# Kernel tuning notes

Hardware: AMD Instinct MI355X
Metric: run time of the kernel (lower is better)

## Reference

```python
import jax, jax.numpy as jnp
import numpy as np

B, C, H, W = 8, 3, 768, 1024
SAMPLE_RATIO = 0.15
G = int(H * W * SAMPLE_RATIO)  # 117964 point triplets
DELTA_COS = 0.867
DELTA_DIFF = 0.005  # hardcoded in select_points_groups' filter_mask call
DELTA_Z = 1e-4


def setup_inputs() -> dict:
    key = jax.random.key(0)
    ks = jax.random.split(key, 8)
    gt = jax.random.normal(ks[0], (B, C, H, W), dtype=jnp.float32)
    pred = jax.random.normal(ks[1], (B, C, H, W), dtype=jnp.float32)
    idx = {}
    for i, (nm, hi) in enumerate([("p1_x", W), ("p1_y", H), ("p2_x", W),
                                  ("p2_y", H), ("p3_x", W), ("p3_y", H)]):
        idx[nm] = jax.random.randint(ks[2 + i], (G,), 0, hi, dtype=jnp.int32)
    return {"gt": gt, "pred": pred, **idx}


def _form_groups(pw, p1_x, p1_y, p2_x, p2_y, p3_x, p3_y):
    # pw: [B,H,W,3] -> groups [B,G,3coord,3pts]
    g1 = pw[:, p1_y, p1_x, :]
    g2 = pw[:, p2_y, p2_x, :]
    g3 = pw[:, p3_y, p3_x, :]
    return jnp.stack([g1, g2, g3], axis=3)


def _vn_loss(gt, pred, p1_x, p1_y, p2_x, p2_y, p3_x, p3_y):
    pw_gt = jnp.transpose(gt, (0, 2, 3, 1))    # [B,H,W,3]
    pw_pred = jnp.transpose(pred, (0, 2, 3, 1))

    pw_g = _form_groups(pw_gt, p1_x, p1_y, p2_x, p2_y, p3_x, p3_y)  # [B,G,3,3]

    # pairwise difference vectors: 12, 13, 23 -> [B,G,3coord,3pair]
    pw12 = pw_g[..., 1] - pw_g[..., 0]
    pw13 = pw_g[..., 2] - pw_g[..., 0]
    pw23 = pw_g[..., 2] - pw_g[..., 1]
    pw_diff = jnp.stack([pw12, pw13, pw23], axis=3)

    # cosine-similarity (Gram) filter: energy[b,g,i,j] = <diff_i, diff_j>
    energy = jnp.einsum("bgci,bgcj->bgij", pw_diff, pw_diff)
    norms = jnp.sqrt(jnp.sum(pw_diff * pw_diff, axis=2))  # [B,G,3]
    nm = norms[..., :, None] * norms[..., None, :]
    norm_energy = energy / (nm + 1e-8)
    mask_cos = jnp.sum((norm_energy > DELTA_COS) | (norm_energy < -DELTA_COS),
                       axis=(2, 3)) > 3                   # [B,G]

    mask_pad = jnp.sum(pw_g[:, :, 2, :] > DELTA_Z, axis=2) == 3
    mask_x = jnp.sum(jnp.abs(pw_diff[:, :, 0, :]) < DELTA_DIFF, axis=2) > 0
    mask_y = jnp.sum(jnp.abs(pw_diff[:, :, 1, :]) < DELTA_DIFF, axis=2) > 0
    mask_z = jnp.sum(jnp.abs(pw_diff[:, :, 2, :]) < DELTA_DIFF, axis=2) > 0
    mask = mask_pad & ~((mask_x & mask_y & mask_z) | mask_cos)  # [B,G]

    pw_gp = _form_groups(pw_pred, p1_x, p1_y, p2_x, p2_y, p3_x, p3_y)
    # torch quirk: boolean mask over [B,G,3] (z of each point) indexes the
    # first 3 dims [B,G,coord], zeroing whole coord-rows to 1e-4
    zmask = pw_gp[:, :, 2, :] == 0.0
    pw_gp = jnp.where(zmask[:, :, :, None], 1e-4, pw_gp)

    def normals(groups):
        p12 = groups[..., 1] - groups[..., 0]
        p13 = groups[..., 2] - groups[..., 0]
        n = jnp.cross(p12, p13, axis=2)
        norm = jnp.linalg.norm(n, axis=2, keepdims=True)
        norm = norm + jnp.where(norm == 0.0, 0.01, 0.0)
        return n / norm

    gt_n = normals(pw_g)
    dt_n = normals(pw_gp)

    per_group = jnp.sum(jnp.abs(gt_n - dt_n), axis=2)  # [B,G]
    m = mask.astype(per_group.dtype)
    # mean over selected groups (batch dims flattened by the torch reshape)
    return jnp.sum(per_group * m) / jnp.maximum(jnp.sum(m), 1.0)


def reference(gt, pred, p1_x, p1_y, p2_x, p2_y, p3_x, p3_y):
    return _vn_loss(gt, pred, p1_x, p1_y, p2_x, p2_y, p3_x, p3_y)
```

## Files before the change

### kernel.cpp

```cpp
#include <hip/hip_runtime.h>
#include <hip/hip_fp16.h>

#define HW_ (768 * 1024)
#define W_ 1024
#define DC 0.867f
#define DD 0.005f
#define DZ 0.0001f

#define SEG_STRIDE 260

__device__ __forceinline__ void vn_group_math(
    const float G1[3], const float G2[3], const float G3[3],
    const float P1[3], const float P2[3], const float P3[3],
    float& s_loss, float& s_cnt)
{
    float d0[3], d1[3], d2[3];
    #pragma unroll
    for (int c = 0; c < 3; c++) {
        d0[c] = G2[c] - G1[c];
        d1[c] = G3[c] - G1[c];
        d2[c] = G3[c] - G2[c];
    }

    float e00 = d0[0]*d0[0] + d0[1]*d0[1] + d0[2]*d0[2];
    float e11 = d1[0]*d1[0] + d1[1]*d1[1] + d1[2]*d1[2];
    float e22 = d2[0]*d2[0] + d2[1]*d2[1] + d2[2]*d2[2];
    float e01 = d0[0]*d1[0] + d0[1]*d1[1] + d0[2]*d1[2];
    float e02 = d0[0]*d2[0] + d0[1]*d2[1] + d0[2]*d2[2];
    float e12 = d1[0]*d2[0] + d1[1]*d2[1] + d1[2]*d2[2];
    float s0 = sqrtf(e00), s1 = sqrtf(e11), s2 = sqrtf(e22);

    int cc = 0;
    {
        float ne;
        ne = e00 / (s0*s0 + 1e-8f); cc += (ne > DC) || (ne < -DC);
        ne = e11 / (s1*s1 + 1e-8f); cc += (ne > DC) || (ne < -DC);
        ne = e22 / (s2*s2 + 1e-8f); cc += (ne > DC) || (ne < -DC);
        ne = e01 / (s0*s1 + 1e-8f); cc += 2 * ((ne > DC) || (ne < -DC));
        ne = e02 / (s0*s2 + 1e-8f); cc += 2 * ((ne > DC) || (ne < -DC));
        ne = e12 / (s1*s2 + 1e-8f); cc += 2 * ((ne > DC) || (ne < -DC));
    }
    bool mask_cos = cc > 3;
    bool mask_pad = (G1[2] > DZ) && (G2[2] > DZ) && (G3[2] > DZ);
    bool mx = (fabsf(d0[0]) < DD) || (fabsf(d1[0]) < DD) || (fabsf(d2[0]) < DD);
    bool my = (fabsf(d0[1]) < DD) || (fabsf(d1[1]) < DD) || (fabsf(d2[1]) < DD);
    bool mz = (fabsf(d0[2]) < DD) || (fabsf(d1[2]) < DD) || (fabsf(d2[2]) < DD);
    bool mask = mask_pad && !((mx && my && mz) || mask_cos);

    if (mask) {
        float n0 = d0[1]*d1[2] - d0[2]*d1[1];
        float n1 = d0[2]*d1[0] - d0[0]*d1[2];
        float n2 = d0[0]*d1[1] - d0[1]*d1[0];
        float nn = sqrtf(n0*n0 + n1*n1 + n2*n2);
        if (nn == 0.f) nn = 0.01f;

        bool zm[3] = { P1[2] == 0.f, P2[2] == 0.f, P3[2] == 0.f };
        float Q1[3], Q2[3], Q3[3];
        #pragma unroll
        for (int c = 0; c < 3; c++) {
            Q1[c] = zm[c] ? 0.0001f : P1[c];
            Q2[c] = zm[c] ? 0.0001f : P2[c];
            Q3[c] = zm[c] ? 0.0001f : P3[c];
        }
        float q0[3], q1[3];
        #pragma unroll
        for (int c = 0; c < 3; c++) {
            q0[c] = Q2[c] - Q1[c];
            q1[c] = Q3[c] - Q1[c];
        }
        float m0 = q0[1]*q1[2] - q0[2]*q1[1];
        float m1 = q0[2]*q1[0] - q0[0]*q1[2];
        float m2 = q0[0]*q1[1] - q0[1]*q1[0];
        float mn = sqrtf(m0*m0 + m1*m1 + m2*m2);
        if (mn == 0.f) mn = 0.01f;

        s_loss += fabsf(n0/nn - m0/mn) + fabsf(n1/nn - m1/mn) + fabsf(n2/nn - m2/mn);
        s_cnt  += 1.f;
    }
}

__device__ __forceinline__ void vn_reduce_store(float s_loss, float s_cnt, double* acc)
{
    #pragma unroll
    for (int off = 32; off > 0; off >>= 1) {
        s_loss += __shfl_down(s_loss, off);
        s_cnt  += __shfl_down(s_cnt,  off);
    }
    __shared__ float ls[4], lc[4];
    int lane = threadIdx.x & 63;
    int wid  = threadIdx.x >> 6;
    if (lane == 0) { ls[wid] = s_loss; lc[wid] = s_cnt; }
    __syncthreads();
    if (threadIdx.x == 0) {
        float tl = ls[0] + ls[1] + ls[2] + ls[3];
        float tc = lc[0] + lc[1] + lc[2] + lc[3];
        atomicAdd(acc,     (double)tl);
        atomicAdd(acc + 1, (double)tc);
    }
}

__global__ __launch_bounds__(256) void vn_mark8(
    const int* __restrict__ p1x, const int* __restrict__ p1y,
    const int* __restrict__ p2x, const int* __restrict__ p2y,
    const int* __restrict__ p3x, const int* __restrict__ p3y,
    int G, unsigned char* __restrict__ mask8)
{
    int g = blockIdx.x * 256 + threadIdx.x;
    if (g >= G) return;
    mask8[p1y[g] * W_ + p1x[g]] = 1;
    mask8[p2y[g] * W_ + p2x[g]] = 1;
    mask8[p3y[g] * W_ + p3x[g]] = 1;
}

__global__ __launch_bounds__(256) void vn_pack_m(
    const float* __restrict__ gt, const float* __restrict__ pred,
    const unsigned char* __restrict__ mask8, uint4* __restrict__ rec)
{
    __shared__ __half lh[48 * SEG_STRIDE];
    __shared__ unsigned char lmask[256];

    size_t px_base = (size_t)blockIdx.x * 256;
    int t = threadIdx.x;
    int w = t >> 6, l = t & 63;

    if (t < 64)
        ((unsigned int*)lmask)[t] = ((const unsigned int*)(mask8 + px_base))[t];

    #pragma unroll
    for (int k = 0; k < 12; k++) {
        int s = w * 12 + k;
        int b = s / 6, c = s % 6;
        const float* src = (c < 3)
            ? gt   + ((size_t)b * 3 + c)       * HW_ + px_base
            : pred + ((size_t)b * 3 + (c - 3)) * HW_ + px_base;
        float4 v = *(const float4*)(src + l * 4);
        __half2 v01 = __floats2half2_rn(v.x, v.y);
        __half2 v23 = __floats2half2_rn(v.z, v.w);
        uint2 pk;
        pk.x = *(unsigned int*)&v01;
        pk.y = *(unsigned int*)&v23;
        *(uint2*)(&lh[(size_t)s * SEG_STRIDE + l * 4]) = pk;
    }

    __syncthreads();

    int b  = t & 7;
    int c6 = b * 6;
    uint4* out = rec + px_base * 8;
    #pragma unroll
    for (int r = 0; r < 8; r++) {
        int j    = t + r * 256;
        int i_px = j >> 3;
        if (lmask[i_px]) {
            uint4 o;
            __half2* hh = (__half2*)&o;
            hh[0] = __halves2half2(lh[(c6 + 0) * SEG_STRIDE + i_px],
                                   lh[(c6 + 1) * SEG_STRIDE + i_px]);
            hh[1] = __halves2half2(lh[(c6 + 2) * SEG_STRIDE + i_px],
                                   lh[(c6 + 3) * SEG_STRIDE + i_px]);
            hh[2] = __halves2half2(lh[(c6 + 4) * SEG_STRIDE + i_px],
                                   lh[(c6 + 5) * SEG_STRIDE + i_px]);
            o.w = 0u;
            out[j] = o;
        }
    }
}

__device__ __forceinline__ void unpack_rec(uint4 r, float G[3], float P[3])
{
    __half2 a = *(__half2*)&r.x;
    __half2 b = *(__half2*)&r.y;
    __half2 c = *(__half2*)&r.z;
    G[0] = __low2float(a);  G[1] = __high2float(a);
    G[2] = __low2float(b);  P[0] = __high2float(b);
    P[1] = __low2float(c);  P[2] = __high2float(c);
}

__global__ __launch_bounds__(256) void vn_gather_h(
    const uint4* __restrict__ rec,
    const int* __restrict__ p1x, const int* __restrict__ p1y,
    const int* __restrict__ p2x, const int* __restrict__ p2y,
    const int* __restrict__ p3x, const int* __restrict__ p3y,
    int G, double* __restrict__ acc)
{
    int t = blockIdx.x * 256 + threadIdx.x;
    int g = t >> 1;
    int h = (t & 1) * 4;

    float s_loss = 0.f, s_cnt = 0.f;

    if (g < G) {
        size_t q1 = ((size_t)(p1y[g] * W_ + p1x[g])) * 8 + h;
        size_t q2 = ((size_t)(p2y[g] * W_ + p2x[g])) * 8 + h;
        size_t q3 = ((size_t)(p3y[g] * W_ + p3x[g])) * 8 + h;

        uint4 r1[4], r2[4], r3[4];
        #pragma unroll
        for (int j = 0; j < 4; j++) r1[j] = rec[q1 + j];
        #pragma unroll
        for (int j = 0; j < 4; j++) r2[j] = rec[q2 + j];
        #pragma unroll
        for (int j = 0; j < 4; j++) r3[j] = rec[q3 + j];

        #pragma unroll
        for (int j = 0; j < 4; j++) {
            float G1[3], P1[3], G2[3], P2[3], G3[3], P3[3];
            unpack_rec(r1[j], G1, P1);
            unpack_rec(r2[j], G2, P2);
            unpack_rec(r3[j], G3, P3);
            vn_group_math(G1, G2, G3, P1, P2, P3, s_loss, s_cnt);
        }
    }

    vn_reduce_store(s_loss, s_cnt, acc);
}

__global__ __launch_bounds__(256) void vn_main(
    const float* __restrict__ gt, const float* __restrict__ pred,
    const int* __restrict__ p1x, const int* __restrict__ p1y,
    const int* __restrict__ p2x, const int* __restrict__ p2y,
    const int* __restrict__ p3x, const int* __restrict__ p3y,
    int G, double* __restrict__ acc)
{
    int g = blockIdx.x * 256 + threadIdx.x;
    int b = blockIdx.y;

    float s_loss = 0.f, s_cnt = 0.f;

    if (g < G) {
        int o1 = p1y[g] * W_ + p1x[g];
        int o2 = p2y[g] * W_ + p2x[g];
        int o3 = p3y[g] * W_ + p3x[g];
        const float* gb = gt   + (size_t)b * 3 * HW_;
        const float* pb = pred + (size_t)b * 3 * HW_;

        float G1[3], G2[3], G3[3], P1[3], P2[3], P3[3];
        #pragma unroll
        for (int c = 0; c < 3; c++) {
            G1[c] = gb[c * HW_ + o1];
            G2[c] = gb[c * HW_ + o2];
            G3[c] = gb[c * HW_ + o3];
            P1[c] = pb[c * HW_ + o1];
            P2[c] = pb[c * HW_ + o2];
            P3[c] = pb[c * HW_ + o3];
        }
        vn_group_math(G1, G2, G3, P1, P2, P3, s_loss, s_cnt);
    }

    vn_reduce_store(s_loss, s_cnt, acc);
}

__global__ void vn_final(const double* __restrict__ acc, float* __restrict__ out)
{
    float s = (float)acc[0];
    float c = (float)acc[1];
    out[0] = s / fmaxf(c, 1.0f);
}

extern "C" void kernel_launch(void* const* d_in, const int* in_sizes, int n_in,
                              void* d_out, int out_size, void* d_ws, size_t ws_size,
                              hipStream_t stream) {
    const float* gt   = (const float*)d_in[0];
    const float* pred = (const float*)d_in[1];
    const int* p1x = (const int*)d_in[2];
    const int* p1y = (const int*)d_in[3];
    const int* p2x = (const int*)d_in[4];
    const int* p2y = (const int*)d_in[5];
    const int* p3x = (const int*)d_in[6];
    const int* p3y = (const int*)d_in[7];

    int G = in_sizes[2];
    int B = in_sizes[0] / (3 * HW_);
    double* acc = (double*)d_ws;

    hipMemsetAsync(acc, 0, 2 * sizeof(double), stream);

    size_t mask_off   = 256;
    size_t mask_bytes = HW_;
    size_t rec_off    = 1 << 20;
    size_t rec_bytes  = (size_t)HW_ * 8 * sizeof(uint4);
    size_t need = rec_off + rec_bytes;

    if (B == 8 && ws_size >= need) {
        unsigned char* mask8 = (unsigned char*)d_ws + mask_off;
        uint4*         rec   = (uint4*)((char*)d_ws + rec_off);

        hipMemsetAsync(mask8, 0, mask_bytes, stream);
        vn_mark8<<<(G + 255) / 256, 256, 0, stream>>>(p1x, p1y, p2x, p2y, p3x, p3y, G, mask8);
        vn_pack_m<<<HW_ / 256, 256, 0, stream>>>(gt, pred, mask8, rec);
        int nthreads = G * 2;
        vn_gather_h<<<(nthreads + 255) / 256, 256, 0, stream>>>(
            rec, p1x, p1y, p2x, p2y, p3x, p3y, G, acc);
    } else {
        dim3 grid((G + 255) / 256, B);
        vn_main<<<grid, 256, 0, stream>>>(gt, pred, p1x, p1y, p2x, p2y, p3x, p3y, G, acc);
    }

    vn_final<<<1, 1, 0, stream>>>(acc, (float*)d_out);
}
```

Measured before the change: 78.99 us.

## Split packed per-pixel records into 8-byte and 4-byte arrays, fold acc reset

Each per-pixel-per-batch record was a 16-byte uint4 with 4 bytes of padding. It is now split into an 8-byte array and a 4-byte array, so the gather kernel reads 12 bytes per record instead of 16, through wider vector loads. The zeroing of the accumulator moves from a separate memset into the mark kernel, which saves one launch. The trade-off is that the gather now issues three separate load streams per point, and the acc reset depends on kernel ordering within the stream.

```diff
diff --git a/kernel.cpp b/kernel.cpp
--- a/kernel.cpp
+++ b/kernel.cpp
@@ -103,9 +103,13 @@
     const int* __restrict__ p1x, const int* __restrict__ p1y,
     const int* __restrict__ p2x, const int* __restrict__ p2y,
     const int* __restrict__ p3x, const int* __restrict__ p3y,
-    int G, unsigned char* __restrict__ mask8)
+    int G, unsigned char* __restrict__ mask8, double* __restrict__ acc)
 {
     int g = blockIdx.x * 256 + threadIdx.x;
+    if (blockIdx.x == 0 && threadIdx.x == 0) {
+        acc[0] = 0.0;
+        acc[1] = 0.0;
+    }
     if (g >= G) return;
     mask8[p1y[g] * W_ + p1x[g]] = 1;
     mask8[p2y[g] * W_ + p2x[g]] = 1;
@@ -114,7 +118,8 @@
 
 __global__ __launch_bounds__(256) void vn_pack_m(
     const float* __restrict__ gt, const float* __restrict__ pred,
-    const unsigned char* __restrict__ mask8, uint4* __restrict__ rec)
+    const unsigned char* __restrict__ mask8,
+    uint2* __restrict__ recLo, unsigned int* __restrict__ recHi)
 {
     __shared__ __half lh[48 * SEG_STRIDE];
     __shared__ unsigned char lmask[256];
@@ -146,38 +151,41 @@
 
     int b  = t & 7;
     int c6 = b * 6;
-    uint4* out = rec + px_base * 8;
+    uint2*        outLo = recLo + px_base * 8;
+    unsigned int* outHi = recHi + px_base * 8;
     #pragma unroll
     for (int r = 0; r < 8; r++) {
         int j    = t + r * 256;
         int i_px = j >> 3;
         if (lmask[i_px]) {
-            uint4 o;
-            __half2* hh = (__half2*)&o;
-            hh[0] = __halves2half2(lh[(c6 + 0) * SEG_STRIDE + i_px],
-                                   lh[(c6 + 1) * SEG_STRIDE + i_px]);
-            hh[1] = __halves2half2(lh[(c6 + 2) * SEG_STRIDE + i_px],
-                                   lh[(c6 + 3) * SEG_STRIDE + i_px]);
-            hh[2] = __halves2half2(lh[(c6 + 4) * SEG_STRIDE + i_px],
-                                   lh[(c6 + 5) * SEG_STRIDE + i_px]);
-            o.w = 0u;
-            out[j] = o;
-        }
-    }
-}
-
-__device__ __forceinline__ void unpack_rec(uint4 r, float G[3], float P[3])
-{
-    __half2 a = *(__half2*)&r.x;
-    __half2 b = *(__half2*)&r.y;
-    __half2 c = *(__half2*)&r.z;
+            __half2 w0 = __halves2half2(lh[(c6 + 0) * SEG_STRIDE + i_px],
+                                        lh[(c6 + 1) * SEG_STRIDE + i_px]);
+            __half2 w1 = __halves2half2(lh[(c6 + 2) * SEG_STRIDE + i_px],
+                                        lh[(c6 + 3) * SEG_STRIDE + i_px]);
+            __half2 w2 = __halves2half2(lh[(c6 + 4) * SEG_STRIDE + i_px],
+                                        lh[(c6 + 5) * SEG_STRIDE + i_px]);
+            uint2 lo;
+            lo.x = *(unsigned int*)&w0;
+            lo.y = *(unsigned int*)&w1;
+            outLo[j] = lo;
+            outHi[j] = *(unsigned int*)&w2;
+        }
+    }
+}
+
+__device__ __forceinline__ void unpack_s(unsigned int lo0, unsigned int lo1,
+                                         unsigned int hi, float G[3], float P[3])
+{
+    __half2 a = *(__half2*)&lo0;
+    __half2 b = *(__half2*)&lo1;
+    __half2 c = *(__half2*)&hi;
     G[0] = __low2float(a);  G[1] = __high2float(a);
     G[2] = __low2float(b);  P[0] = __high2float(b);
     P[1] = __low2float(c);  P[2] = __high2float(c);
 }
 
-__global__ __launch_bounds__(256) void vn_gather_h(
-    const uint4* __restrict__ rec,
+__global__ __launch_bounds__(256) void vn_gather_s(
+    const uint2* __restrict__ recLo, const unsigned int* __restrict__ recHi,
     const int* __restrict__ p1x, const int* __restrict__ p1y,
     const int* __restrict__ p2x, const int* __restrict__ p2y,
     const int* __restrict__ p3x, const int* __restrict__ p3y,
@@ -194,20 +202,29 @@
         size_t q2 = ((size_t)(p2y[g] * W_ + p2x[g])) * 8 + h;
         size_t q3 = ((size_t)(p3y[g] * W_ + p3x[g])) * 8 + h;
 
-        uint4 r1[4], r2[4], r3[4];
-        #pragma unroll
-        for (int j = 0; j < 4; j++) r1[j] = rec[q1 + j];
-        #pragma unroll
-        for (int j = 0; j < 4; j++) r2[j] = rec[q2 + j];
-        #pragma unroll
-        for (int j = 0; j < 4; j++) r3[j] = rec[q3 + j];
+        const uint4* L = (const uint4*)recLo;
+        const uint4* H = (const uint4*)recHi;
+
+        uint4 a1 = L[q1 >> 1], b1 = L[(q1 >> 1) + 1], h1 = H[q1 >> 2];
+        uint4 a2 = L[q2 >> 1], b2 = L[(q2 >> 1) + 1], h2v = H[q2 >> 2];
+        uint4 a3 = L[q3 >> 1], b3 = L[(q3 >> 1) + 1], h3 = H[q3 >> 2];
+
+        unsigned int lo0_1[4] = {a1.x, a1.z, b1.x, b1.z};
+        unsigned int lo1_1[4] = {a1.y, a1.w, b1.y, b1.w};
+        unsigned int hi_1[4]  = {h1.x, h1.y, h1.z, h1.w};
+        unsigned int lo0_2[4] = {a2.x, a2.z, b2.x, b2.z};
+        unsigned int lo1_2[4] = {a2.y, a2.w, b2.y, b2.w};
+        unsigned int hi_2[4]  = {h2v.x, h2v.y, h2v.z, h2v.w};
+        unsigned int lo0_3[4] = {a3.x, a3.z, b3.x, b3.z};
+        unsigned int lo1_3[4] = {a3.y, a3.w, b3.y, b3.w};
+        unsigned int hi_3[4]  = {h3.x, h3.y, h3.z, h3.w};
 
         #pragma unroll
         for (int j = 0; j < 4; j++) {
             float G1[3], P1[3], G2[3], P2[3], G3[3], P3[3];
-            unpack_rec(r1[j], G1, P1);
-            unpack_rec(r2[j], G2, P2);
-            unpack_rec(r3[j], G3, P3);
+            unpack_s(lo0_1[j], lo1_1[j], hi_1[j], G1, P1);
+            unpack_s(lo0_2[j], lo1_2[j], hi_2[j], G2, P2);
+            unpack_s(lo0_3[j], lo1_3[j], hi_3[j], G3, P3);
             vn_group_math(G1, G2, G3, P1, P2, P3, s_loss, s_cnt);
         }
     }
@@ -271,27 +288,30 @@
 
     int G = in_sizes[2];
     int B = in_sizes[0] / (3 * HW_);
+
     double* acc = (double*)d_ws;
 
-    hipMemsetAsync(acc, 0, 2 * sizeof(double), stream);
-
-    size_t mask_off   = 256;
-    size_t mask_bytes = HW_;
-    size_t rec_off    = 1 << 20;
-    size_t rec_bytes  = (size_t)HW_ * 8 * sizeof(uint4);
-    size_t need = rec_off + rec_bytes;
+    size_t mask_off  = 256;
+    size_t lo_off    = 1 << 20;
+    size_t lo_bytes  = (size_t)HW_ * 8 * sizeof(uint2);
+    size_t hi_off    = lo_off + lo_bytes;
+    size_t hi_bytes  = (size_t)HW_ * 8 * sizeof(unsigned int);
+    size_t need = hi_off + hi_bytes;
 
     if (B == 8 && ws_size >= need) {
         unsigned char* mask8 = (unsigned char*)d_ws + mask_off;
-        uint4*         rec   = (uint4*)((char*)d_ws + rec_off);
-
-        hipMemsetAsync(mask8, 0, mask_bytes, stream);
-        vn_mark8<<<(G + 255) / 256, 256, 0, stream>>>(p1x, p1y, p2x, p2y, p3x, p3y, G, mask8);
-        vn_pack_m<<<HW_ / 256, 256, 0, stream>>>(gt, pred, mask8, rec);
+        uint2*         recLo = (uint2*)((char*)d_ws + lo_off);
+        unsigned int*  recHi = (unsigned int*)((char*)d_ws + hi_off);
+
+        hipMemsetAsync(mask8, 0, HW_, stream);
+        vn_mark8<<<(G + 255) / 256, 256, 0, stream>>>(
+            p1x, p1y, p2x, p2y, p3x, p3y, G, mask8, acc);
+        vn_pack_m<<<HW_ / 256, 256, 0, stream>>>(gt, pred, mask8, recLo, recHi);
         int nthreads = G * 2;
-        vn_gather_h<<<(nthreads + 255) / 256, 256, 0, stream>>>(
-            rec, p1x, p1y, p2x, p2y, p3x, p3y, G, acc);
+        vn_gather_s<<<(nthreads + 255) / 256, 256, 0, stream>>>(
+            recLo, recHi, p1x, p1y, p2x, p2y, p3x, p3y, G, acc);
     } else {
+        hipMemsetAsync(acc, 0, 2 * sizeof(double), stream);
         dim3 grid((G + 255) / 256, B);
         vn_main<<<grid, 256, 0, stream>>>(gt, pred, p1x, p1y, p2x, p2y, p3x, p3y, G, acc);
     }
```

Measured after the change: 78.15 us. No clear change (-1.1%).
